# Optimization experiments

Hardware: AMD Instinct MI355X
Metric: run time of the kernel (lower is better)

## Reference

```python
import jax, jax.numpy as jnp
import numpy as np

B, P, D, N, H = 1, 256, 512, 8, 64
STD = 0.02
IGNORE = -1000000.0


def setup_inputs() -> dict:
    key = jax.random.key(0)
    ks = jax.random.split(key, 9)
    inp = {"normalized_resid_pre": jax.random.normal(ks[0], (B, P, D), jnp.float32)}
    for i, s in enumerate("ABCDE"):
        inp["W_" + s] = STD * jax.random.normal(ks[i + 1], (N, D, H), jnp.float32)
        inp["b_" + s] = jnp.zeros((N, H), jnp.float32)
    inp["W_V"] = STD * jax.random.normal(ks[6], (N, H, H, H), jnp.float32)
    inp["W_K"] = STD * jax.random.normal(ks[7], (N, H, H, H), jnp.float32)
    inp["W_O"] = STD * jax.random.normal(ks[8], (N, H, D), jnp.float32)
    inp["b_O"] = jnp.zeros((D,), jnp.float32)
    return inp


def reference(normalized_resid_pre, W_A, b_A, W_B, b_B, W_C, b_C, W_D, b_D, W_E, b_E, W_V, W_K, W_O, b_O):
    x = normalized_resid_pre
    b_sz = x.shape[0]
    proj = lambda W, b: jnp.einsum('ndh,bpd->bpnh', W, x) + b
    ta = proj(W_A, b_A)
    tb = proj(W_B, b_B)
    tc = proj(W_C, b_C)
    td = proj(W_D, b_D)
    te = proj(W_E, b_E)
    # V_Layer: v[b, p1, p2, n, h3]
    v = jnp.einsum('bpnh,bqng,nhgf->bpqnf', td, te, W_V)
    # TrittentionCScore: chained einsums -> scores[b, n, p, q, r]
    step1 = jnp.einsum('brnk,nijk->brij', tc, W_K)
    step2 = jnp.einsum('brij,bqnj->briq', step1, tb)
    scores = jnp.einsum('briq,bpni->bnpqr', step2, ta)
    # CausalMask (attn_eq=False, order_attn=True): mask over (t=p, s=q, q=r) dims
    ti = jnp.arange(P)[:, None, None]
    si = jnp.arange(P)[None, :, None]
    qi = jnp.arange(P)[None, None, :]
    mask = (ti >= qi) | (si >= qi) | (ti >= si)  # [P, P, P]
    scores = jnp.where(mask, IGNORE, scores)
    # TrittentionCPattern: b n p q r -> b n r (p q), /d_head, extra column, softmax
    flat = jnp.transpose(scores, (0, 1, 4, 2, 3)).reshape(b_sz, N, P, P * P) / H
    extra = jnp.full((b_sz, N, P, 1), -1000.0, flat.dtype)
    attn = jax.nn.softmax(jnp.concatenate([flat, extra], axis=-1), axis=-1)
    # Z_Layer: v -> b n h (p s), extra zero column, combine
    vf = jnp.transpose(v, (0, 3, 4, 1, 2)).reshape(b_sz, N, H, P * P)
    vf = jnp.concatenate([vf, jnp.zeros((b_sz, N, H, 1), vf.dtype)], axis=-1)
    z = jnp.einsum('bnql,bnhl->bqnh', attn, vf)
    # Result + Out
    zint = jnp.einsum('bqnh,nhd->bqnd', z, W_O)
    return zint.sum(axis=2) + b_O
```

## Files before the change

kernel.cpp:

```cpp
#include <hip/hip_runtime.h>
#include <hip/hip_bf16.h>


typedef __hip_bfloat16 bf16;
typedef __attribute__((ext_vector_type(8))) short short8;
typedef __attribute__((ext_vector_type(4))) short s16x4;
typedef __attribute__((ext_vector_type(4))) float floatx4;

__device__ __forceinline__ float ldf(const float* p){ return *p; }
__device__ __forceinline__ float ldf(const bf16* p){ return __bfloat162float(*p); }
__device__ __forceinline__ void  stf(float* p, float v){ *p = v; }
__device__ __forceinline__ void  stf(bf16*  p, float v){ *p = __float2bfloat16(v); }

__device__ __forceinline__ floatx4 mfma16(short8 a, short8 b, floatx4 c){
  return __builtin_amdgcn_mfma_f32_16x16x32_bf16(a, b, c, 0, 0, 0);
}
__device__ __forceinline__ short8 ld_g8(const bf16* p){
  return *reinterpret_cast<const short8*>(p);
}
__device__ __forceinline__ short bfs(float x){
  bf16 v = __float2bfloat16(x);
  return *reinterpret_cast<short*>(&v);
}

__device__ __forceinline__ void ld4(const bf16* p, float* o){
  s16x4 v = *reinterpret_cast<const s16x4*>(p);
  #pragma unroll
  for (int i = 0; i < 4; i++)
    o[i] = __uint_as_float(((unsigned)(unsigned short)v[i]) << 16);
}
__device__ __forceinline__ void ld4(const float* p, float* o){
  float4 v = *reinterpret_cast<const float4*>(p);
  o[0] = v.x; o[1] = v.y; o[2] = v.z; o[3] = v.w;
}

__device__ __forceinline__ bool is_bf16_x(const void* xv)
{
  const unsigned* x32 = (const unsigned*)xv;
  unsigned w = x32[threadIdx.x & 63];
  unsigned lo = w & 0xFFFFu;
  unsigned e  = (lo >> 7) & 0xFFu;
  bool v = (lo == 0u) || (e >= 90u && e <= 145u);
  unsigned long long m = __ballot(v);
  return __popcll(m) >= 40;
}

template<typename TI>
__device__ __forceinline__ void proj_body(
    const TI* __restrict__ x, const TI* const* Ws, const TI* const* bs,
    bf16* __restrict__ tproj, float* As, float* Bs)
{
  const int bz = blockIdx.z, j = bz >> 3, n = bz & 7;
  const TI* B    = Ws[j] + (size_t)n * 32768;
  const TI* bias = bs[j] + n * 64;
  bf16* out = tproj + (size_t)j * 131072;
  const int m0 = blockIdx.y * 64;
  const int t = threadIdx.x, tx = t & 15, ty = t >> 4;
  float acc[4][4] = {};
  for (int k0 = 0; k0 < 512; k0 += 16) {
    { int m = t >> 2, kk = (t & 3) * 4;
      float a[4]; ld4(x + (size_t)(m0 + m) * 512 + (k0 + kk), a);
      As[(kk+0)*68+m] = a[0]; As[(kk+1)*68+m] = a[1];
      As[(kk+2)*68+m] = a[2]; As[(kk+3)*68+m] = a[3]; }
    { int kk = t >> 4, nn = (t & 15) * 4;
      float b[4]; ld4(B + (size_t)(k0 + kk) * 64 + nn, b);
      Bs[kk*68+nn+0] = b[0]; Bs[kk*68+nn+1] = b[1];
      Bs[kk*68+nn+2] = b[2]; Bs[kk*68+nn+3] = b[3]; }
    __syncthreads();
    #pragma unroll
    for (int kk = 0; kk < 16; kk++) {
      float4 a4 = *reinterpret_cast<const float4*>(&As[kk*68 + ty*4]);
      float4 b4 = *reinterpret_cast<const float4*>(&Bs[kk*68 + tx*4]);
      float av[4] = {a4.x,a4.y,a4.z,a4.w}, bv[4] = {b4.x,b4.y,b4.z,b4.w};
      #pragma unroll
      for (int im = 0; im < 4; im++)
        #pragma unroll
        for (int in = 0; in < 4; in++) acc[im][in] += av[im] * bv[in];
    }
    __syncthreads();
  }
  #pragma unroll
  for (int im = 0; im < 4; im++)
    #pragma unroll
    for (int in = 0; in < 4; in++) {
      float v = acc[im][in] + ldf(bias + tx*4 + in);
      int p = m0 + ty*4 + im, h = tx*4 + in;
      if (j < 3) out[(size_t)p * 512 + n*64 + h] = __float2bfloat16(v);
      else       out[(size_t)n * 16384 + (size_t)h * 256 + p] = __float2bfloat16(v);
    }
}

__global__ __launch_bounds__(256) void proj_all(
    const void* __restrict__ x,
    const void* W0, const void* b0, const void* W1, const void* b1,
    const void* W2, const void* b2, const void* W3, const void* b3,
    const void* W4, const void* b4, bf16* __restrict__ tproj,
    const void* __restrict__ WKf, bf16* __restrict__ wkbf)
{
  __shared__ float As[16*68];
  __shared__ float Bs[16*68];
  const int bz = blockIdx.z;
  if (bz >= 40) {
    if (is_bf16_x(x)) return;
    const float* src = (const float*)WKf;
    const int cb = (bz - 40) * 4 + blockIdx.y;
    for (size_t i = ((size_t)cb*256 + threadIdx.x)*8; i < 2097152;
         i += (size_t)96*256*8) {
      float4 u0 = *reinterpret_cast<const float4*>(src + i);
      float4 u1 = *reinterpret_cast<const float4*>(src + i + 4);
      s16x4 lo = {bfs(u0.x), bfs(u0.y), bfs(u0.z), bfs(u0.w)};
      s16x4 hi = {bfs(u1.x), bfs(u1.y), bfs(u1.z), bfs(u1.w)};
      *reinterpret_cast<s16x4*>(wkbf + i)     = lo;
      *reinterpret_cast<s16x4*>(wkbf + i + 4) = hi;
    }
    return;
  }
  if (is_bf16_x(x)) {
    const bf16* Ws[5] = {(const bf16*)W0,(const bf16*)W1,(const bf16*)W2,
                         (const bf16*)W3,(const bf16*)W4};
    const bf16* bs[5] = {(const bf16*)b0,(const bf16*)b1,(const bf16*)b2,
                         (const bf16*)b3,(const bf16*)b4};
    proj_body<bf16>((const bf16*)x, Ws, bs, tproj, As, Bs);
  } else {
    const float* Ws[5] = {(const float*)W0,(const float*)W1,(const float*)W2,
                          (const float*)W3,(const float*)W4};
    const float* bs[5] = {(const float*)b0,(const float*)b1,(const float*)b2,
                          (const float*)b3,(const float*)b4};
    proj_body<float>((const float*)x, Ws, bs, tproj, As, Bs);
  }
}

__device__ __forceinline__ void s1t_body(
    const bf16* __restrict__ tc, const bf16* __restrict__ WK,
    bf16* __restrict__ s1t)
{
  const int i = blockIdx.x;
  const int t = threadIdx.x, wid = t >> 6, lane = t & 63, quad = lane >> 4, l16 = lane & 15;
  const int rw = blockIdx.y * 64 + wid * 16;
  floatx4 acc[4];
  #pragma unroll
  for (int jt = 0; jt < 4; jt++) acc[jt] = (floatx4){0.f, 0.f, 0.f, 0.f};
  for (int kc = 0; kc < 16; kc++) {
    short8 af = ld_g8(tc + (size_t)(rw + l16) * 512 + kc*32 + quad*8);
    const int n = kc >> 1, kk = (kc & 1) * 32 + quad * 8;
    #pragma unroll
    for (int jt = 0; jt < 4; jt++) {
      short8 bf = ld_g8(WK + ((size_t)(n*64 + i) * 64 + jt*16 + l16) * 64 + kk);
      acc[jt] = mfma16(af, bf, acc[jt]);
    }
  }
  #pragma unroll
  for (int jt = 0; jt < 4; jt++)
    #pragma unroll
    for (int reg = 0; reg < 4; reg++)
      s1t[(size_t)(rw + quad*4 + reg) * 4096 + i*64 + jt*16 + l16] =
          __float2bfloat16(acc[jt][reg]);
}

__global__ __launch_bounds__(256) void s1t_all(
    const void* __restrict__ x, const bf16* __restrict__ tb,
    const bf16* __restrict__ tc, const void* __restrict__ WK_orig,
    const bf16* __restrict__ wkbf,
    bf16* __restrict__ tbsbf, bf16* __restrict__ s1t)
{
  if (blockIdx.y == 4) {
    int t = blockIdx.x * 256 + threadIdx.x;
    int q = t >> 6, j = t & 63;
    float s = 0.f;
    #pragma unroll
    for (int n = 0; n < 8; n++) s += ldf(tb + q*512 + n*64 + j);
    tbsbf[t] = __float2bfloat16(s * 0.015625f);
    return;
  }
  const bf16* wk = is_bf16_x(x) ? (const bf16*)WK_orig : wkbf;
  s1t_body(tc, wk, s1t);
}

#define E_PHASE(PT, BUF)                                                      \
  {                                                                           \
    const int ptb_ = ((PT)*4 + wid) * 16;                                     \
    for (int qt2 = 0; qt2 < 2; qt2++) {                                       \
      const int qh = qc + qt2*16;                                             \
      char* erow0 = (BUF) + (quad*4)*72 + (qt2*16 + l16)*2;                   \
      if (qh + 15 <= ptb_) {                                                  \
        for (int reg = 0; reg < 4; reg++)                                     \
          *reinterpret_cast<bf16*>(erow0 + reg*72) = __float2bfloat16(0.f);   \
      } else {                                                                \
        floatx4 acc = {0.f, 0.f, 0.f, 0.f};                                   \
        acc = mfma16(taf[PT][0], cfr[qt2][0], acc);                           \
        acc = mfma16(taf[PT][1], cfr[qt2][1], acc);                           \
        if (qh >= ptb_ + 16 && qh + 15 < r) {                                 \
          for (int reg = 0; reg < 4; reg++) {                                 \
            float e = __expf(acc[reg]);                                       \
            Zp += e;                                                          \
            *reinterpret_cast<bf16*>(erow0 + reg*72) = __float2bfloat16(e);   \
          }                                                                   \
        } else {                                                              \
          for (int reg = 0; reg < 4; reg++) {                                 \
            int p = ptb_ + quad*4 + reg;                                      \
            int q = qh + l16;                                                 \
            float e = (p < q && q < r) ? __expf(acc[reg]) : 0.f;              \
            Zp += e;                                                          \
            *reinterpret_cast<bf16*>(erow0 + reg*72) = __float2bfloat16(e);   \
          }                                                                   \
        }                                                                     \
      }                                                                       \
    }                                                                         \
  }

__global__ __launch_bounds__(256) void tri_attn(
    const bf16* __restrict__ ta,
    const bf16* __restrict__ tbsbf,
    const bf16* __restrict__ s1t,
    const bf16* __restrict__ tdT,
    const bf16* __restrict__ teT,
    bf16* __restrict__ Sbuf)
{
  __shared__ __align__(16) char smb[44544];
  const int bx = blockIdx.x;
  const int n = bx & 7;
  const int r = 255 - (bx >> 3);
  const int t = threadIdx.x;
  const int wid = t >> 6, lane = t & 63, quad = lane >> 4, l16 = lane & 15;
  bf16* srow = Sbuf + (size_t)n * 1048576 + (size_t)r * 4096;
  if (r < 2) {
    short8 zz = (short8){0,0,0,0,0,0,0,0};
    reinterpret_cast<short8*>(srow)[t]       = zz;
    reinterpret_cast<short8*>(srow)[t + 256] = zz;
    return;
  }
  const int nch  = ((r - 1) >> 5) + 1;
  const int rcap = nch * 32;

  {
    const bf16* s1r = s1t + (size_t)r * 4096;
    short8 bfr[4][2];
    #pragma unroll
    for (int it = 0; it < 4; it++)
      #pragma unroll
      for (int kc = 0; kc < 2; kc++)
        bfr[it][kc] = ld_g8(s1r + (it*16 + l16)*64 + kc*32 + quad*8);
    #pragma unroll
    for (int qt = 0; qt < 4; qt++) {
      const int q0 = wid * 64 + qt * 16;
      if (q0 >= rcap) continue;
      if (q0 >= r) {
        #pragma unroll
        for (int it = 0; it < 4; it++)
          #pragma unroll
          for (int reg = 0; reg < 4; reg++) {
            int q = q0 + quad*4 + reg;
            *reinterpret_cast<bf16*>(smb + q*136 + (it*16 + l16)*2) =
                __float2bfloat16(0.f);
          }
        continue;
      }
      short8 af0 = ld_g8(tbsbf + (q0 + l16)*64 + quad*8);
      short8 af1 = ld_g8(tbsbf + (q0 + l16)*64 + 32 + quad*8);
      #pragma unroll
      for (int it = 0; it < 4; it++) {
        floatx4 acc = {0.f, 0.f, 0.f, 0.f};
        acc = mfma16(af0, bfr[it][0], acc);
        acc = mfma16(af1, bfr[it][1], acc);
        #pragma unroll
        for (int reg = 0; reg < 4; reg++) {
          int q = q0 + quad*4 + reg;
          float v = (q >= 1 && q < r) ? acc[reg] : 0.f;
          *reinterpret_cast<bf16*>(smb + q*136 + (it*16 + l16)*2) = __float2bfloat16(v);
        }
      }
    }
  }
  short8 taf[4][2];
  #pragma unroll
  for (int pt = 0; pt < 4; pt++)
    #pragma unroll
    for (int kc = 0; kc < 2; kc++)
      taf[pt][kc] = ld_g8(ta + (size_t)((pt*4 + wid)*16 + l16)*512 + n*64
                             + kc*32 + quad*8);
  __syncthreads();

  floatx4 Tacc[4][4];
  #pragma unroll
  for (int pt = 0; pt < 4; pt++)
    #pragma unroll
    for (int gt = 0; gt < 4; gt++) Tacc[pt][gt] = (floatx4){0.f, 0.f, 0.f, 0.f};
  float Zp = 0.f;
  char* bufA = smb + 34816 + wid * 2304;
  char* bufB = bufA + 1152;
  for (int ch = 0; ch < nch; ch++) {
    const int qc = ch * 32;
    if (qc + 31 <= wid * 16) continue;
    short8 cfr[2][2];
    #pragma unroll
    for (int qt2 = 0; qt2 < 2; qt2++)
      #pragma unroll
      for (int kc = 0; kc < 2; kc++)
        cfr[qt2][kc] = *reinterpret_cast<const short8*>(
            smb + (qc + qt2*16 + l16)*136 + (kc*32 + quad*8)*2);
    short8 tef[4];
    #pragma unroll
    for (int gt = 0; gt < 4; gt++)
      tef[gt] = ld_g8(teT + (size_t)n*16384 + (gt*16 + l16)*256 + qc + quad*8);

    {
      const bool alive0 = ((0*4 + wid)*16 < qc + 31);
      const bool alive1 = ((1*4 + wid)*16 < qc + 31);
      short8 ef0, ef1;
      if (alive0) { E_PHASE(0, bufA)
                    ef0 = *reinterpret_cast<const short8*>(bufA + l16*72 + quad*16); }
      if (alive1) { E_PHASE(1, bufB)
                    ef1 = *reinterpret_cast<const short8*>(bufB + l16*72 + quad*16); }
      if (alive0) { __builtin_amdgcn_s_setprio(1);
        #pragma unroll
        for (int gt = 0; gt < 4; gt++) Tacc[0][gt] = mfma16(ef0, tef[gt], Tacc[0][gt]);
        __builtin_amdgcn_s_setprio(0); }
      if (alive1) { __builtin_amdgcn_s_setprio(1);
        #pragma unroll
        for (int gt = 0; gt < 4; gt++) Tacc[1][gt] = mfma16(ef1, tef[gt], Tacc[1][gt]);
        __builtin_amdgcn_s_setprio(0); }
    }
    {
      const bool alive2 = ((2*4 + wid)*16 < qc + 31);
      const bool alive3 = ((3*4 + wid)*16 < qc + 31);
      short8 ef2, ef3;
      if (alive2) { E_PHASE(2, bufA)
                    ef2 = *reinterpret_cast<const short8*>(bufA + l16*72 + quad*16); }
      if (alive3) { E_PHASE(3, bufB)
                    ef3 = *reinterpret_cast<const short8*>(bufB + l16*72 + quad*16); }
      if (alive2) { __builtin_amdgcn_s_setprio(1);
        #pragma unroll
        for (int gt = 0; gt < 4; gt++) Tacc[2][gt] = mfma16(ef2, tef[gt], Tacc[2][gt]);
        __builtin_amdgcn_s_setprio(0); }
      if (alive3) { __builtin_amdgcn_s_setprio(1);
        #pragma unroll
        for (int gt = 0; gt < 4; gt++) Tacc[3][gt] = mfma16(ef3, tef[gt], Tacc[3][gt]);
        __builtin_amdgcn_s_setprio(0); }
    }
  }
  #pragma unroll
  for (int off = 32; off; off >>= 1) Zp += __shfl_down(Zp, off);
  float* scr = reinterpret_cast<float*>(smb + 44032);
  if (lane == 0) scr[wid] = Zp;
  __syncthreads();
  const float rinv = 1.f / (scr[0] + scr[1] + scr[2] + scr[3]);

  #pragma unroll
  for (int pt = 0; pt < 4; pt++) {
    if ((pt*4 + wid)*16 >= rcap) continue;
    #pragma unroll
    for (int gt = 0; gt < 4; gt++)
      #pragma unroll
      for (int reg = 0; reg < 4; reg++) {
        int g = gt*16 + l16;
        int p = (pt*4 + wid)*16 + quad*4 + reg;
        *reinterpret_cast<bf16*>(smb + g*528 + p*2) = __float2bfloat16(Tacc[pt][gt][reg]);
      }
  }
  __syncthreads();

  {
    short8 Taf[8];
    #pragma unroll
    for (int kc = 0; kc < 8; kc++)
      if (kc < nch)
        Taf[kc] = *reinterpret_cast<const short8*>(
            smb + (wid*16 + l16)*528 + (kc*32 + quad*8)*2);
    #pragma unroll
    for (int ht = 0; ht < 4; ht++) {
      floatx4 acc = {0.f, 0.f, 0.f, 0.f};
      __builtin_amdgcn_s_setprio(1);
      #pragma unroll
      for (int kc = 0; kc < 8; kc++) {
        if (kc < nch) {
          short8 bfragd = ld_g8(tdT + (size_t)n*16384 + (ht*16 + l16)*256 + kc*32 + quad*8);
          acc = mfma16(Taf[kc], bfragd, acc);
        }
      }
      __builtin_amdgcn_s_setprio(0);
      #pragma unroll
      for (int reg = 0; reg < 4; reg++) {
        int g = wid*16 + quad*4 + reg, h = ht*16 + l16;
        srow[h*64 + g] = __float2bfloat16(acc[reg] * rinv);
      }
    }
  }
}

template<typename TW>
__device__ __forceinline__ void z_body(
    const bf16* __restrict__ Sbuf, const TW* __restrict__ WV,
    float* __restrict__ zpart, int kslice, char* lds)
{
  const int rt = blockIdx.x, n = blockIdx.y, ks = blockIdx.z;
  const int t = threadIdx.x, wid = t >> 6, lane = t & 63, quad = lane >> 4, l16 = lane & 15;
  const int rw = rt * 16;
  const int k0 = ks * kslice;
  const TW*  wvn = WV   + (size_t)n * 262144;
  const bf16* sn = Sbuf + (size_t)n * 1048576;
  floatx4 acc = {0.f, 0.f, 0.f, 0.f};
  const int row = t >> 3, f8 = (t & 7) * 8;
  for (int kb = k0; kb < k0 + kslice; kb += 32) {
    { const TW* src = wvn + (size_t)(kb + row) * 64 + f8;
      short sv[8];
      if constexpr (sizeof(TW) == 2) {
        short8 v = ld_g8((const bf16*)src);
        #pragma unroll
        for (int j = 0; j < 8; j++) sv[j] = v[j];
      } else {
        float4 a = *reinterpret_cast<const float4*>(src);
        float4 b = *reinterpret_cast<const float4*>(src + 4);
        sv[0]=bfs(a.x); sv[1]=bfs(a.y); sv[2]=bfs(a.z); sv[3]=bfs(a.w);
        sv[4]=bfs(b.x); sv[5]=bfs(b.y); sv[6]=bfs(b.z); sv[7]=bfs(b.w);
      }
      short* dst = reinterpret_cast<short*>(lds + row*136 + f8*2);
      s16x4 lo = {sv[0],sv[1],sv[2],sv[3]}, hi = {sv[4],sv[5],sv[6],sv[7]};
      *reinterpret_cast<s16x4*>(dst)     = lo;
      *reinterpret_cast<s16x4*>(dst + 4) = hi;
    }
    __syncthreads();
    short8 af = ld_g8(sn + (size_t)(rw + l16) * 4096 + kb + quad*8);
    short8 bfv;
    #pragma unroll
    for (int j = 0; j < 8; j++)
      bfv[j] = *reinterpret_cast<const short*>(
          lds + (quad*8 + j)*136 + (wid*16 + l16)*2);
    acc = mfma16(af, bfv, acc);
    __syncthreads();
  }
  float* zp = zpart + (size_t)ks * 131072;
  #pragma unroll
  for (int reg = 0; reg < 4; reg++)
    zp[(size_t)(rw + quad*4 + reg) * 512 + n*64 + wid*16 + l16] = acc[reg];
}

__global__ __launch_bounds__(256) void z_all(
    const void* __restrict__ x, const bf16* __restrict__ Sbuf,
    const void* __restrict__ WV, float* __restrict__ zpart, int kslice)
{
  __shared__ __align__(16) char lds[32 * 136];
  if (is_bf16_x(x)) z_body<bf16>(Sbuf, (const bf16*)WV, zpart, kslice, lds);
  else              z_body<float>(Sbuf, (const float*)WV, zpart, kslice, lds);
}

__global__ __launch_bounds__(256) void zred_kern(
    const float* __restrict__ zpart, bf16* __restrict__ zbb, int ks)
{
  int idx = blockIdx.x * 256 + threadIdx.x;
  float s = 0.f;
  for (int k = 0; k < ks; k++) s += zpart[(size_t)k * 131072 + idx];
  zbb[idx] = __float2bfloat16(s);
}

template<typename TB, typename TC>
__device__ __forceinline__ void gemm_body(
    const bf16* __restrict__ A, const TB* __restrict__ B, TC* __restrict__ C,
    const TB* __restrict__ bias, float* As, float* Bs)
{
  const int m0 = blockIdx.y * 32, n0 = blockIdx.x * 32;
  const int t = threadIdx.x, tx = t & 15, ty = t >> 4;
  float acc[2][2] = {};
  for (int k0 = 0; k0 < 512; k0 += 16) {
    { int m = t >> 3, kk = (t & 7) * 2;
      const bf16* ap = A + (size_t)(m0 + m) * 512 + (k0 + kk);
      As[(kk+0)*34+m] = ldf(ap+0); As[(kk+1)*34+m] = ldf(ap+1); }
    { int kk = t >> 4, nn = (t & 15) * 2;
      const TB* bp = B + (size_t)(k0 + kk) * 512 + (n0 + nn);
      Bs[kk*34+nn+0] = ldf(bp+0); Bs[kk*34+nn+1] = ldf(bp+1); }
    __syncthreads();
    #pragma unroll
    for (int kk = 0; kk < 16; kk++) {
      float a0 = As[kk*34 + ty*2], a1 = As[kk*34 + ty*2 + 1];
      float b0 = Bs[kk*34 + tx*2], b1 = Bs[kk*34 + tx*2 + 1];
      acc[0][0] += a0*b0; acc[0][1] += a0*b1;
      acc[1][0] += a1*b0; acc[1][1] += a1*b1;
    }
    __syncthreads();
  }
  #pragma unroll
  for (int im = 0; im < 2; im++) {
    TC* cp = C + (size_t)(m0 + ty*2 + im) * 512 + n0 + tx*2;
    #pragma unroll
    for (int in = 0; in < 2; in++) {
      float v = acc[im][in] + ldf(bias + n0 + tx*2 + in);
      stf(cp + in, v);
    }
  }
}

__global__ __launch_bounds__(256) void gemm_all(
    const void* __restrict__ x, const bf16* __restrict__ zbb,
    const void* __restrict__ WO, const void* __restrict__ bO,
    void* __restrict__ out)
{
  __shared__ float As[16*34];
  __shared__ float Bs[16*34];
  if (is_bf16_x(x))
    gemm_body<bf16, bf16>(zbb, (const bf16*)WO, (bf16*)out, (const bf16*)bO, As, Bs);
  else
    gemm_body<float, float>(zbb, (const float*)WO, (float*)out, (const float*)bO, As, Bs);
}

extern "C" void kernel_launch(void* const* d_in, const int* in_sizes, int n_in,
                              void* d_out, int out_size, void* d_ws, size_t ws_size,
                              hipStream_t stream)
{
  (void)in_sizes; (void)n_in; (void)out_size;
  char* wsb = (char*)d_ws;
  bf16* tproj = (bf16*)(wsb + 256);
  bf16* tbsbf = (bf16*)(wsb + 1310976);
  bf16* s1t   = (bf16*)(wsb + 1343744);
  bf16* zbb   = (bf16*)(wsb + 3440896);
  bf16* Sbuf  = (bf16*)(wsb + 4194304);
  bf16* wkbf  = (bf16*)(wsb + 4194304);
  const long TE = 131072;
  const bool bigws = (ws_size == 0) || (ws_size >= 25165824);
  const int  ks     = bigws ? 8 : 2;
  const int  kslice = 4096 / ks;
  float* zpart = (float*)(bigws ? (wsb + 20971520) : (wsb + 1343744));

  proj_all<<<dim3(1,4,64), 256, 0, stream>>>(
      d_in[0], d_in[1], d_in[2], d_in[3], d_in[4], d_in[5], d_in[6],
      d_in[7], d_in[8], d_in[9], d_in[10], tproj, d_in[12], wkbf);
  s1t_all<<<dim3(64,5), 256, 0, stream>>>(
      d_in[0], tproj + 1*TE, tproj + 2*TE, d_in[12], wkbf, tbsbf, s1t);
  tri_attn<<<2048, 256, 0, stream>>>(
      tproj, tbsbf, s1t, tproj + 3*TE, tproj + 4*TE, Sbuf);
  z_all<<<dim3(16,8,ks), 256, 0, stream>>>(
      d_in[0], Sbuf, d_in[11], zpart, kslice);
  zred_kern<<<512, 256, 0, stream>>>(zpart, zbb, ks);
  gemm_all<<<dim3(16,8), 256, 0, stream>>>(
      d_in[0], zbb, d_in[13], d_in[14], d_out);
}
```

Before: 237.3 us.

## Pre-transpose W_V to bf16 in projection kernel and use LDS-free Z matmul

Adds extra blocks to the projection kernel that convert W_V to bf16 and transpose it so the reduction dimension is contiguous. A new Z kernel then reads both operands straight from global memory into MFMA fragments, with no shared-memory staging, and the K-split drops from 8 to 4. zpart moves into the smaller workspace region so the transposed W_V can occupy the large one. The aim is cheaper Z-stage loads and less partial-sum reduction, at the cost of extra transpose work in the first kernel and uncoalesced strided global loads.

```diff
diff --git a/kernel.cpp b/kernel.cpp
--- a/kernel.cpp
+++ b/kernel.cpp
@@ -95,16 +95,54 @@
     const void* W0, const void* b0, const void* W1, const void* b1,
     const void* W2, const void* b2, const void* W3, const void* b3,
     const void* W4, const void* b4, bf16* __restrict__ tproj,
-    const void* __restrict__ WKf, bf16* __restrict__ wkbf)
-{
-  __shared__ float As[16*68];
-  __shared__ float Bs[16*68];
-  const int bz = blockIdx.z;
+    const void* __restrict__ WKf, bf16* __restrict__ wkbf,
+    const void* __restrict__ WVin, bf16* __restrict__ WVT)
+{
+  __shared__ __align__(16) char shm[8704];
+  float* As = (float*)shm;
+  float* Bs = (float*)(shm + 4352);
+  short (*tileS)[68] = (short(*)[68])shm;
+  const int bz = blockIdx.z, t = threadIdx.x;
+  if (bz >= 64) {
+    const bool bfp = is_bf16_x(x);
+    const int cb = (bz - 64) * 4 + blockIdx.y;
+    for (int tile = cb*4; tile < cb*4 + 4; tile++) {
+      const int n = tile >> 6, kg = tile & 63;
+      { int kr = t >> 2, f16 = (t & 3) * 16;
+        if (bfp) {
+          const bf16* src = (const bf16*)WVin + ((size_t)n*4096 + kg*64 + kr)*64 + f16;
+          *reinterpret_cast<short8*>(&tileS[kr][f16])     = ld_g8(src);
+          *reinterpret_cast<short8*>(&tileS[kr][f16 + 8]) = ld_g8(src + 8);
+        } else {
+          const float* src = (const float*)WVin + ((size_t)n*4096 + kg*64 + kr)*64 + f16;
+          float4 u0 = *reinterpret_cast<const float4*>(src);
+          float4 u1 = *reinterpret_cast<const float4*>(src + 4);
+          float4 u2 = *reinterpret_cast<const float4*>(src + 8);
+          float4 u3 = *reinterpret_cast<const float4*>(src + 12);
+          short8 w0 = {bfs(u0.x),bfs(u0.y),bfs(u0.z),bfs(u0.w),
+                       bfs(u1.x),bfs(u1.y),bfs(u1.z),bfs(u1.w)};
+          short8 w1 = {bfs(u2.x),bfs(u2.y),bfs(u2.z),bfs(u2.w),
+                       bfs(u3.x),bfs(u3.y),bfs(u3.z),bfs(u3.w)};
+          *reinterpret_cast<short8*>(&tileS[kr][f16])     = w0;
+          *reinterpret_cast<short8*>(&tileS[kr][f16 + 8]) = w1;
+        } }
+      __syncthreads();
+      { int fr = t >> 2, k16 = (t & 3) * 16;
+        short8 w0, w1;
+        #pragma unroll
+        for (int j = 0; j < 8; j++) { w0[j] = tileS[k16+j][fr]; w1[j] = tileS[k16+8+j][fr]; }
+        bf16* dst = WVT + ((size_t)n*64 + fr)*4096 + kg*64 + k16;
+        *reinterpret_cast<short8*>(dst)     = w0;
+        *reinterpret_cast<short8*>(dst + 8) = w1; }
+      __syncthreads();
+    }
+    return;
+  }
   if (bz >= 40) {
     if (is_bf16_x(x)) return;
     const float* src = (const float*)WKf;
     const int cb = (bz - 40) * 4 + blockIdx.y;
-    for (size_t i = ((size_t)cb*256 + threadIdx.x)*8; i < 2097152;
+    for (size_t i = ((size_t)cb*256 + t)*8; i < 2097152;
          i += (size_t)96*256*8) {
       float4 u0 = *reinterpret_cast<const float4*>(src + i);
       float4 u1 = *reinterpret_cast<const float4*>(src + i + 4);
@@ -387,6 +425,29 @@
   }
 }
 
+__global__ __launch_bounds__(256) void zmm_kern(
+    const bf16* __restrict__ Sbuf, const bf16* __restrict__ WVT,
+    float* __restrict__ zpart, int kslice)
+{
+  const int rt = blockIdx.x, n = blockIdx.y, ks = blockIdx.z;
+  const int t = threadIdx.x, wid = t >> 6, lane = t & 63, quad = lane >> 4, l16 = lane & 15;
+  const int rw = rt * 16;
+  const bf16* sn  = Sbuf + (size_t)n * 1048576 + (size_t)(rw + l16) * 4096;
+  const bf16* wvf = WVT + ((size_t)n*64 + wid*16 + l16) * 4096;
+  floatx4 acc = {0.f, 0.f, 0.f, 0.f};
+  const int k0 = ks * kslice;
+  #pragma unroll 4
+  for (int kb = k0; kb < k0 + kslice; kb += 32) {
+    short8 af = ld_g8(sn + kb + quad*8);
+    short8 bf = ld_g8(wvf + kb + quad*8);
+    acc = mfma16(af, bf, acc);
+  }
+  float* zp = zpart + (size_t)ks * 131072;
+  #pragma unroll
+  for (int reg = 0; reg < 4; reg++)
+    zp[(size_t)(rw + quad*4 + reg) * 512 + n*64 + wid*16 + l16] = acc[reg];
+}
+
 template<typename TW>
 __device__ __forceinline__ void z_body(
     const bf16* __restrict__ Sbuf, const TW* __restrict__ WV,
@@ -513,21 +574,27 @@
   bf16* zbb   = (bf16*)(wsb + 3440896);
   bf16* Sbuf  = (bf16*)(wsb + 4194304);
   bf16* wkbf  = (bf16*)(wsb + 4194304);
+  bf16* WVT   = (bf16*)(wsb + 20971520);
+  float* zpart = (float*)(wsb + 1343744);
   const long TE = 131072;
   const bool bigws = (ws_size == 0) || (ws_size >= 25165824);
-  const int  ks     = bigws ? 8 : 2;
+  const int  ks     = bigws ? 4 : 2;
   const int  kslice = 4096 / ks;
-  float* zpart = (float*)(bigws ? (wsb + 20971520) : (wsb + 1343744));
-
-  proj_all<<<dim3(1,4,64), 256, 0, stream>>>(
+
+  proj_all<<<dim3(1,4, bigws ? 96 : 64), 256, 0, stream>>>(
       d_in[0], d_in[1], d_in[2], d_in[3], d_in[4], d_in[5], d_in[6],
-      d_in[7], d_in[8], d_in[9], d_in[10], tproj, d_in[12], wkbf);
+      d_in[7], d_in[8], d_in[9], d_in[10], tproj, d_in[12], wkbf,
+      d_in[11], WVT);
   s1t_all<<<dim3(64,5), 256, 0, stream>>>(
       d_in[0], tproj + 1*TE, tproj + 2*TE, d_in[12], wkbf, tbsbf, s1t);
   tri_attn<<<2048, 256, 0, stream>>>(
       tproj, tbsbf, s1t, tproj + 3*TE, tproj + 4*TE, Sbuf);
-  z_all<<<dim3(16,8,ks), 256, 0, stream>>>(
-      d_in[0], Sbuf, d_in[11], zpart, kslice);
+  if (bigws) {
+    zmm_kern<<<dim3(16,8,4), 256, 0, stream>>>(Sbuf, WVT, zpart, kslice);
+  } else {
+    z_all<<<dim3(16,8,2), 256, 0, stream>>>(
+        d_in[0], Sbuf, d_in[11], zpart, kslice);
+  }
   zred_kern<<<512, 256, 0, stream>>>(zpart, zbb, ks);
   gemm_all<<<dim3(16,8), 256, 0, stream>>>(
       d_in[0], zbb, d_in[13], d_in[14], d_out);
```

Result: no change. 238.0 us (+0.3%).
